# Kernel optimization log

Measured on AMD Instinct MI355X. Metric: run time of the kernel, lower is better.

## Reference

```python
import jax, jax.numpy as jnp
import numpy as np

D_MODEL = 2048
NUM_HEADS = 16
D_HEAD = D_MODEL // NUM_HEADS
MAX_SEQ_LEN = 2048
THETA = 10000.0


def setup_inputs() -> dict:
    key = jax.random.key(0)
    kx, kq, kk, kv, ko = jax.random.split(key, 5)
    std = float(np.sqrt(2.0 / (D_MODEL + D_MODEL)))
    def tn(k):
        # truncated normal in [-3std, 3std] scaled by std
        return std * jax.random.truncated_normal(k, -3.0, 3.0, (D_MODEL, D_MODEL), jnp.float32)
    return {
        "x": jax.random.normal(kx, (2, MAX_SEQ_LEN, D_MODEL), jnp.float32),
        "w_q": tn(kq),
        "w_k": tn(kk),
        "w_v": tn(kv),
        "w_o": tn(ko),
    }


def _rope(x):
    # x: [B, H, S, Dh], default positions = arange(S)
    S = x.shape[-2]
    pos = jnp.arange(S, dtype=jnp.float32)
    inv_freq = 1.0 / (THETA ** (jnp.arange(0, D_HEAD, 2, dtype=jnp.float32) / D_HEAD))
    ang = pos[:, None] * inv_freq[None, :]           # [S, Dh/2]
    cos = jnp.cos(ang).astype(x.dtype)
    sin = jnp.sin(ang).astype(x.dtype)
    x_even = x[..., 0::2]
    x_odd = x[..., 1::2]
    out_even = x_even * cos - x_odd * sin
    out_odd = x_even * sin + x_odd * cos
    # interleave even/odd back
    return jnp.stack([out_even, out_odd], axis=-1).reshape(x.shape)


def reference(x, w_q, w_k, w_v, w_o):
    B, S, _ = x.shape
    def split_heads(t):
        return t.reshape(B, S, NUM_HEADS, D_HEAD).transpose(0, 2, 1, 3)  # [B,H,S,Dh]
    q = split_heads(x @ w_q.T)
    k = split_heads(x @ w_k.T)
    v = split_heads(x @ w_v.T)
    q = _rope(q)
    k = _rope(k)
    scores = jnp.einsum('bhqd,bhkd->bhqk', q, k) / jnp.sqrt(jnp.asarray(D_HEAD, x.dtype))
    causal = jnp.tril(jnp.ones((S, S), dtype=bool))
    scores = jnp.where(causal, scores, jnp.finfo(scores.dtype).min)
    attn = jax.nn.softmax(scores, axis=-1)
    out = jnp.einsum('bhqk,bhkd->bhqd', attn, v)     # [B,H,S,Dh]
    out = out.transpose(0, 2, 1, 3).reshape(B, S, D_MODEL)
    return out @ w_o.T
```

## Files before the change

### kernel.cpp

```cpp
#include <hip/hip_runtime.h>
#include <hip/hip_bf16.h>

typedef __bf16 bf16;
typedef __bf16 bf16x8 __attribute__((ext_vector_type(8)));
typedef __bf16 bf16x4 __attribute__((ext_vector_type(4)));
typedef float f32x4 __attribute__((ext_vector_type(4)));

#define MFMA_BF16(a, b, c) __builtin_amdgcn_mfma_f32_16x16x32_bf16(a, b, c, 0, 0, 0)

constexpr int D_MODEL = 2048;
constexpr int NUM_HEADS = 16;
constexpr int D_HEAD = 128;
constexpr int SEQ = 2048;
constexpr int BATCH = 2;
constexpr int M_TOTAL = BATCH * SEQ;

__device__ __forceinline__ void gld_lds16(const bf16* g, bf16* l) {
  __builtin_amdgcn_global_load_lds((const __attribute__((address_space(1))) void*)g,
                                   (__attribute__((address_space(3))) void*)l, 16, 0, 0);
}

__global__ __launch_bounds__(256) void cvt_all(const float* __restrict__ x,
                                               const float* __restrict__ wq,
                                               const float* __restrict__ wk,
                                               const float* __restrict__ wv,
                                               const float* __restrict__ wo,
                                               bf16* __restrict__ dst) {
  const long i = (long)blockIdx.x * 256 + threadIdx.x;
  const float* src;
  long off;
  if (i < 2097152) {
    src = x; off = i;
  } else {
    const long j = i - 2097152;
    const int w = (int)(j >> 20);
    off = j & 1048575;
    src = (w == 0) ? wq : (w == 1) ? wk : (w == 2) ? wv : wo;
  }
  float4 v = reinterpret_cast<const float4*>(src)[off];
  bf16x4 o;
  o[0] = (bf16)v.x; o[1] = (bf16)v.y; o[2] = (bf16)v.z; o[3] = (bf16)v.w;
  reinterpret_cast<bf16x4*>(dst)[i] = o;
}

enum { EP_F32 = 0, EP_QKV = 1 };

template <int EPI>
__global__ __launch_bounds__(512, 2) void gemm_bt(const bf16* __restrict__ A,
                                                  const bf16* __restrict__ B,
                                                  void* __restrict__ C0,
                                                  void* __restrict__ C1,
                                                  void* __restrict__ C2,
                                                  int M, int N, int K) {
  __shared__ __align__(16) bf16 As[3][256 * 32];
  __shared__ __align__(16) bf16 Bs[3][256 * 32];
  const int tid = threadIdx.x;
  const int lane = tid & 63;
  const int wave = tid >> 6;
  const int lane15 = lane & 15;
  const int quad = lane >> 4;

  const int nwg = gridDim.x;
  const int cpx = nwg >> 3;
  const int swz = (blockIdx.x & 7) * cpx + (blockIdx.x >> 3);
  const int NBX = N >> 8;
  const int m0 = (swz / NBX) * 256;
  const int n0 = (swz % NBX) * 256;

  const int wm = (wave >> 2) * 128;
  const int wn = (wave & 3) * 64;

  const int arow = wave * 16 + (lane >> 2);
  const int achk = ((lane & 3) ^ (arow & 3)) * 8;
  long a_off[2], b_off[2];
#pragma unroll
  for (int i = 0; i < 2; ++i) {
    a_off[i] = (long)(m0 + i * 128 + arow) * K + achk;
    b_off[i] = (long)(n0 + i * 128 + arow) * K + achk;
  }
  const int dstoff = wave * 512;

  const int ca = (quad ^ (lane15 & 3)) * 8;

  f32x4 acc[8][4];
#pragma unroll
  for (int i = 0; i < 8; ++i)
#pragma unroll
    for (int j = 0; j < 4; ++j) acc[i][j] = (f32x4){0.f, 0.f, 0.f, 0.f};

  const int NT = K >> 5;

#pragma unroll
  for (int i = 0; i < 2; ++i) gld_lds16(A + a_off[i], &As[0][i * 4096 + dstoff]);
#pragma unroll
  for (int i = 0; i < 2; ++i) gld_lds16(B + b_off[i], &Bs[0][i * 4096 + dstoff]);
#pragma unroll
  for (int i = 0; i < 2; ++i) gld_lds16(A + a_off[i] + 32, &As[1][i * 4096 + dstoff]);
#pragma unroll
  for (int i = 0; i < 2; ++i) gld_lds16(B + b_off[i] + 32, &Bs[1][i * 4096 + dstoff]);
  asm volatile("s_waitcnt vmcnt(4)" ::: "memory");
  __builtin_amdgcn_s_barrier();
  __builtin_amdgcn_sched_barrier(0);

  int bcur = 0, bstg = 2;
  for (int t = 0; t < NT; ++t) {
    const bf16* Ab = As[bcur];
    const bf16* Bb = Bs[bcur];
    const long kst = (long)(t + 2) * 32;
    const bool st = (t + 2 < NT);

    bf16x8 bfrg[4], afrg[4];
#pragma unroll
    for (int j = 0; j < 4; ++j)
      bfrg[j] = *reinterpret_cast<const bf16x8*>(&Bb[(wn + j * 16 + lane15) * 32 + ca]);
#pragma unroll
    for (int i = 0; i < 4; ++i)
      afrg[i] = *reinterpret_cast<const bf16x8*>(&Ab[(wm + i * 16 + lane15) * 32 + ca]);
    if (st) {
      gld_lds16(A + a_off[0] + kst, &As[bstg][dstoff]);
      gld_lds16(A + a_off[1] + kst, &As[bstg][4096 + dstoff]);
    }
    __builtin_amdgcn_s_barrier();
    __builtin_amdgcn_sched_barrier(0);
    __builtin_amdgcn_s_setprio(1);
#pragma unroll
    for (int i = 0; i < 4; ++i)
#pragma unroll
      for (int j = 0; j < 4; ++j) acc[i][j] = MFMA_BF16(afrg[i], bfrg[j], acc[i][j]);
    __builtin_amdgcn_s_setprio(0);

    bf16x8 afr2[4];
#pragma unroll
    for (int i = 0; i < 4; ++i)
      afr2[i] = *reinterpret_cast<const bf16x8*>(&Ab[(wm + (i + 4) * 16 + lane15) * 32 + ca]);
    if (st) {
      gld_lds16(B + b_off[0] + kst, &Bs[bstg][dstoff]);
      gld_lds16(B + b_off[1] + kst, &Bs[bstg][4096 + dstoff]);
      asm volatile("s_waitcnt vmcnt(4)" ::: "memory");
    } else if (t == NT - 2) {
      asm volatile("s_waitcnt vmcnt(0)" ::: "memory");
    }
    __builtin_amdgcn_s_barrier();
    __builtin_amdgcn_sched_barrier(0);
    __builtin_amdgcn_s_setprio(1);
#pragma unroll
    for (int i = 0; i < 4; ++i)
#pragma unroll
      for (int j = 0; j < 4; ++j) acc[i + 4][j] = MFMA_BF16(afr2[i], bfrg[j], acc[i + 4][j]);
    __builtin_amdgcn_s_setprio(0);

    __builtin_amdgcn_s_barrier();
    __builtin_amdgcn_sched_barrier(0);
    bstg = bcur;
    bcur = (bcur == 2) ? 0 : bcur + 1;
  }

  if (EPI == EP_F32) {
#pragma unroll
    for (int i = 0; i < 8; ++i)
#pragma unroll
      for (int j = 0; j < 4; ++j)
#pragma unroll
        for (int r = 0; r < 4; ++r) {
          const int m = m0 + wm + i * 16 + quad * 4 + r;
          const int n = n0 + wn + j * 16 + lane15;
          reinterpret_cast<float*>(C0)[(long)m * N + n] = acc[i][j][r];
        }
  } else {
    const int mat = n0 >> 11;
    bf16* dst = (mat == 0) ? (bf16*)C0 : (mat == 1) ? (bf16*)C1 : (bf16*)C2;
    const int nb = n0 & 2047;
    if (mat < 2) {
#pragma unroll
      for (int i = 0; i < 8; ++i)
#pragma unroll
        for (int j = 0; j < 4; ++j)
#pragma unroll
          for (int r = 0; r < 4; ++r) {
            const int m = m0 + wm + i * 16 + quad * 4 + r;
            const int nl = nb + wn + j * 16 + lane15;
            const int b = m >> 11;
            const int s = m & (SEQ - 1);
            const int h = nl >> 7;
            const int d = nl & (D_HEAD - 1);
            float v = acc[i][j][r];
            float other = __shfl_xor(v, 1);
            float fr = exp2f((float)(d & ~1) * -0.103810253f);
            float ang = (float)s * fr;
            float sn = __sinf(ang);
            float cs = __cosf(ang);
            float outv = (lane15 & 1) ? (v * cs + other * sn) : (v * cs - other * sn);
            dst[(((long)(b * NUM_HEADS + h)) * SEQ + s) * D_HEAD + d] = (bf16)outv;
          }
    } else {
#pragma unroll
      for (int i = 0; i < 8; ++i)
#pragma unroll
        for (int j = 0; j < 4; ++j) {
          bf16x4 pk;
#pragma unroll
          for (int r = 0; r < 4; ++r) pk[r] = (bf16)acc[i][j][r];
          const int m = m0 + wm + i * 16 + quad * 4;
          const int b = m >> 11;
          const int s = m & (SEQ - 1);
          const int nl = nb + wn + j * 16 + lane15;
          const int h = nl >> 7;
          const int d = nl & (D_HEAD - 1);
          *reinterpret_cast<bf16x4*>(
              &dst[(((long)(b * NUM_HEADS + h)) * D_HEAD + d) * SEQ + s]) = pk;
        }
    }
  }
}

__global__ __launch_bounds__(256) void flash_attn(const bf16* __restrict__ Q,
                                                  const bf16* __restrict__ K,
                                                  const bf16* __restrict__ Vt,
                                                  bf16* __restrict__ O) {
  __shared__ __align__(16) bf16 Kl[2][64 * 128];
  __shared__ __align__(16) bf16 Vl[2][128 * 64];
  __shared__ __align__(16) bf16 P[4 * 16 * 72];
  const int tid = threadIdx.x;
  const int lane = tid & 63;
  const int wave = tid >> 6;
  const int lane15 = lane & 15;
  const int quad = lane >> 4;
  const int idx = blockIdx.x >> 3;
  const int bh = (blockIdx.x & 7) * 4 + (idx & 3);
  const int qcg = 31 - (idx >> 2);
  const int q0 = qcg * 64 + wave * 16;
  const long base = (long)bh * SEQ * D_HEAD;
  const bf16* qp = Q + base;
  const bf16* kp = K + base;
  const bf16* vp = Vt + base;
  bf16* Pw = &P[wave * 16 * 72];
  constexpr float scale = 0.08838834764831845f;
  constexpr float SMAX = 30.0f;

  int ksrc[4], vsrc[4];
  const int kdst = wave * 512;
#pragma unroll
  for (int i = 0; i < 4; ++i) {
    const int c = i * 256 + tid;
    const int krow = c >> 4;
    ksrc[i] = krow * D_HEAD + (((c & 15) ^ (krow & 15)) * 8);
    const int vd = c >> 3;
    vsrc[i] = vd * SEQ + (((c & 7) ^ (vd & 7)) * 8);
  }

  bf16x8 bq[4];
#pragma unroll
  for (int kk = 0; kk < 4; ++kk)
    bq[kk] = *reinterpret_cast<const bf16x8*>(qp + (long)(q0 + lane15) * D_HEAD + kk * 32 + quad * 8);

  f32x4 o_acc[8];
#pragma unroll
  for (int dj = 0; dj < 8; ++dj) o_acc[dj] = (f32x4){0.f, 0.f, 0.f, 0.f};
  float l_part = 0.f;
  const int qcol = q0 + lane15;

  const int nkt = qcg + 1;

#pragma unroll
  for (int i = 0; i < 4; ++i) gld_lds16(kp + ksrc[i], &Kl[0][i * 2048 + kdst]);
#pragma unroll
  for (int i = 0; i < 4; ++i) gld_lds16(vp + vsrc[i], &Vl[0][i * 2048 + kdst]);
  __syncthreads();

  for (int kt = 0; kt < nkt; ++kt) {
    const int k0 = kt * 64;
    const int buf = kt & 1;

    if (kt + 1 < nkt) {
      const int nk0 = k0 + 64;
#pragma unroll
      for (int i = 0; i < 4; ++i) gld_lds16(kp + nk0 * D_HEAD + ksrc[i], &Kl[buf ^ 1][i * 2048 + kdst]);
#pragma unroll
      for (int i = 0; i < 4; ++i) gld_lds16(vp + nk0 + vsrc[i], &Vl[buf ^ 1][i * 2048 + kdst]);
    }

    f32x4 sc[4];
#pragma unroll
    for (int j = 0; j < 4; ++j) sc[j] = (f32x4){0.f, 0.f, 0.f, 0.f};
#pragma unroll
    for (int j = 0; j < 4; ++j) {
#pragma unroll
      for (int kk = 0; kk < 4; ++kk) {
        bf16x8 ak = *reinterpret_cast<const bf16x8*>(
            &Kl[buf][(j * 16 + lane15) * D_HEAD + (((kk * 4 + quad) ^ lane15) * 8)]);
        sc[j] = MFMA_BF16(ak, bq[kk], sc[j]);
      }
    }

#pragma unroll
    for (int j = 0; j < 4; ++j) {
      bf16x4 pk;
#pragma unroll
      for (int r = 0; r < 4; ++r) {
        const int kpos = k0 + j * 16 + quad * 4 + r;
        float p = (kpos <= qcol) ? __expf(sc[j][r] * scale - SMAX) : 0.f;
        l_part += p;
        pk[r] = (bf16)p;
      }
      *reinterpret_cast<bf16x4*>(&Pw[lane15 * 72 + j * 16 + quad * 4]) = pk;
    }

#pragma unroll
    for (int kc = 0; kc < 2; ++kc) {
      bf16x8 ap = *reinterpret_cast<const bf16x8*>(&Pw[lane15 * 72 + kc * 32 + quad * 8]);
#pragma unroll
      for (int dj = 0; dj < 8; ++dj) {
        bf16x8 bv = *reinterpret_cast<const bf16x8*>(
            &Vl[buf][(dj * 16 + lane15) * 64 + (((kc * 4 + quad) ^ (lane15 & 7)) * 8)]);
        o_acc[dj] = MFMA_BF16(ap, bv, o_acc[dj]);
      }
    }

    __syncthreads();
  }

  float lsum = l_part;
  lsum += __shfl_xor(lsum, 16);
  lsum += __shfl_xor(lsum, 32);

  const int b = bh >> 4;
  const int h = bh & 15;
#pragma unroll
  for (int r = 0; r < 4; ++r) {
    const float lr = __shfl(lsum, quad * 4 + r);
    const float inv_l = 1.0f / lr;
    const int qrow = q0 + quad * 4 + r;
#pragma unroll
    for (int dj = 0; dj < 8; ++dj)
      O[((long)b * SEQ + qrow) * D_MODEL + h * D_HEAD + dj * 16 + lane15] =
          (bf16)(o_acc[dj][r] * inv_l);
  }
}

extern "C" void kernel_launch(void* const* d_in, const int* in_sizes, int n_in,
                              void* d_out, int out_size, void* d_ws, size_t ws_size,
                              hipStream_t stream) {
  const float* x = (const float*)d_in[0];
  const float* wq = (const float*)d_in[1];
  const float* wk = (const float*)d_in[2];
  const float* wv = (const float*)d_in[3];
  const float* wo = (const float*)d_in[4];
  float* out = (float*)d_out;

  char* ws = (char*)d_ws;
  size_t off = 0;
  bf16* x_bf = (bf16*)(ws + off);  off += (size_t)M_TOTAL * D_MODEL * 2;
  bf16* wq_bf = (bf16*)(ws + off); off += (size_t)D_MODEL * D_MODEL * 2;
  bf16* wk_bf = (bf16*)(ws + off); off += (size_t)D_MODEL * D_MODEL * 2;
  bf16* wv_bf = (bf16*)(ws + off); off += (size_t)D_MODEL * D_MODEL * 2;
  bf16* wo_bf = (bf16*)(ws + off); off += (size_t)D_MODEL * D_MODEL * 2;
  bf16* q_r = (bf16*)(ws + off);   off += (size_t)M_TOTAL * D_MODEL * 2;
  bf16* k_r = (bf16*)(ws + off);   off += (size_t)M_TOTAL * D_MODEL * 2;
  bf16* vt_r = (bf16*)(ws + off);  off += (size_t)M_TOTAL * D_MODEL * 2;
  bf16* a_o = (bf16*)(ws + off);   off += (size_t)M_TOTAL * D_MODEL * 2;

  cvt_all<<<24576, dim3(256), 0, stream>>>(x, wq, wk, wv, wo, x_bf);

  gemm_bt<EP_QKV><<<dim3((M_TOTAL / 256) * (3 * D_MODEL / 256)), dim3(512), 0, stream>>>(
      x_bf, wq_bf, q_r, k_r, vt_r, M_TOTAL, 3 * D_MODEL, D_MODEL);

  flash_attn<<<dim3(1024), dim3(256), 0, stream>>>(q_r, k_r, vt_r, a_o);

  gemm_bt<EP_F32><<<dim3((M_TOTAL / 256) * (D_MODEL / 256)), dim3(512), 0, stream>>>(
      a_o, wo_bf, out, nullptr, nullptr, M_TOTAL, D_MODEL, D_MODEL);
}
```

Baseline: 388.2 us.

## Template GEMM on M-tile, use 128-row tiles for output projection, simplify pipeline

Makes the GEMM kernel's M tile a template parameter. The output projection now uses 128-row tiles, which doubles its block count so the grid fills all CUs on the device. The main loop is restructured: all A and B prefetches are issued together, and the two half-MFMA phases with their intermediate barriers are collapsed into one phase. The LDS swizzle pattern is also changed. In exchange, register pressure rises in the 256-row instantiation, and the output GEMM loses some reuse of B per block.

```diff
diff --git a/kernel.cpp b/kernel.cpp
--- a/kernel.cpp
+++ b/kernel.cpp
@@ -45,14 +45,16 @@
 
 enum { EP_F32 = 0, EP_QKV = 1 };
 
-template <int EPI>
+template <int EPI, int BM>
 __global__ __launch_bounds__(512, 2) void gemm_bt(const bf16* __restrict__ A,
                                                   const bf16* __restrict__ B,
                                                   void* __restrict__ C0,
                                                   void* __restrict__ C1,
                                                   void* __restrict__ C2,
                                                   int M, int N, int K) {
-  __shared__ __align__(16) bf16 As[3][256 * 32];
+  constexpr int MFR = BM / 32;
+  constexpr int AI = BM / 128;
+  __shared__ __align__(16) bf16 As[3][BM * 32];
   __shared__ __align__(16) bf16 Bs[3][256 * 32];
   const int tid = threadIdx.x;
   const int lane = tid & 63;
@@ -64,41 +66,44 @@
   const int cpx = nwg >> 3;
   const int swz = (blockIdx.x & 7) * cpx + (blockIdx.x >> 3);
   const int NBX = N >> 8;
-  const int m0 = (swz / NBX) * 256;
+  const int m0 = (swz / NBX) * BM;
   const int n0 = (swz % NBX) * 256;
 
-  const int wm = (wave >> 2) * 128;
+  const int wm = (wave >> 2) * (BM / 2);
   const int wn = (wave & 3) * 64;
 
-  const int arow = wave * 16 + (lane >> 2);
-  const int achk = ((lane & 3) ^ (arow & 3)) * 8;
+  const int arow = tid >> 2;
+  const int achk = ((tid & 3) ^ ((arow >> 1) & 3)) * 8;
   long a_off[2], b_off[2];
 #pragma unroll
-  for (int i = 0; i < 2; ++i) {
-    a_off[i] = (long)(m0 + i * 128 + arow) * K + achk;
-    b_off[i] = (long)(n0 + i * 128 + arow) * K + achk;
-  }
+  for (int i = 0; i < AI; ++i) a_off[i] = (long)(m0 + i * 128 + arow) * K + achk;
+#pragma unroll
+  for (int i = 0; i < 2; ++i) b_off[i] = (long)(n0 + i * 128 + arow) * K + achk;
   const int dstoff = wave * 512;
 
-  const int ca = (quad ^ (lane15 & 3)) * 8;
-
-  f32x4 acc[8][4];
-#pragma unroll
-  for (int i = 0; i < 8; ++i)
+  const int ca = (quad ^ ((lane15 >> 1) & 3)) * 8;
+
+  f32x4 acc[MFR][4];
+#pragma unroll
+  for (int i = 0; i < MFR; ++i)
 #pragma unroll
     for (int j = 0; j < 4; ++j) acc[i][j] = (f32x4){0.f, 0.f, 0.f, 0.f};
 
   const int NT = K >> 5;
 
 #pragma unroll
-  for (int i = 0; i < 2; ++i) gld_lds16(A + a_off[i], &As[0][i * 4096 + dstoff]);
+  for (int i = 0; i < AI; ++i) gld_lds16(A + a_off[i], &As[0][i * 4096 + dstoff]);
 #pragma unroll
   for (int i = 0; i < 2; ++i) gld_lds16(B + b_off[i], &Bs[0][i * 4096 + dstoff]);
 #pragma unroll
-  for (int i = 0; i < 2; ++i) gld_lds16(A + a_off[i] + 32, &As[1][i * 4096 + dstoff]);
+  for (int i = 0; i < AI; ++i) gld_lds16(A + a_off[i] + 32, &As[1][i * 4096 + dstoff]);
 #pragma unroll
   for (int i = 0; i < 2; ++i) gld_lds16(B + b_off[i] + 32, &Bs[1][i * 4096 + dstoff]);
-  asm volatile("s_waitcnt vmcnt(4)" ::: "memory");
+  if constexpr (BM == 256) {
+    asm volatile("s_waitcnt vmcnt(4)" ::: "memory");
+  } else {
+    asm volatile("s_waitcnt vmcnt(3)" ::: "memory");
+  }
   __builtin_amdgcn_s_barrier();
   __builtin_amdgcn_sched_barrier(0);
 
@@ -109,46 +114,37 @@
     const long kst = (long)(t + 2) * 32;
     const bool st = (t + 2 < NT);
 
-    bf16x8 bfrg[4], afrg[4];
+    bf16x8 bfrg[4], afrg[MFR];
 #pragma unroll
     for (int j = 0; j < 4; ++j)
       bfrg[j] = *reinterpret_cast<const bf16x8*>(&Bb[(wn + j * 16 + lane15) * 32 + ca]);
 #pragma unroll
-    for (int i = 0; i < 4; ++i)
+    for (int i = 0; i < MFR; ++i)
       afrg[i] = *reinterpret_cast<const bf16x8*>(&Ab[(wm + i * 16 + lane15) * 32 + ca]);
+
     if (st) {
-      gld_lds16(A + a_off[0] + kst, &As[bstg][dstoff]);
-      gld_lds16(A + a_off[1] + kst, &As[bstg][4096 + dstoff]);
-    }
-    __builtin_amdgcn_s_barrier();
-    __builtin_amdgcn_sched_barrier(0);
+#pragma unroll
+      for (int i = 0; i < AI; ++i) gld_lds16(A + a_off[i] + kst, &As[bstg][i * 4096 + dstoff]);
+#pragma unroll
+      for (int i = 0; i < 2; ++i) gld_lds16(B + b_off[i] + kst, &Bs[bstg][i * 4096 + dstoff]);
+    }
+
     __builtin_amdgcn_s_setprio(1);
 #pragma unroll
-    for (int i = 0; i < 4; ++i)
+    for (int i = 0; i < MFR; ++i)
 #pragma unroll
       for (int j = 0; j < 4; ++j) acc[i][j] = MFMA_BF16(afrg[i], bfrg[j], acc[i][j]);
     __builtin_amdgcn_s_setprio(0);
 
-    bf16x8 afr2[4];
-#pragma unroll
-    for (int i = 0; i < 4; ++i)
-      afr2[i] = *reinterpret_cast<const bf16x8*>(&Ab[(wm + (i + 4) * 16 + lane15) * 32 + ca]);
     if (st) {
-      gld_lds16(B + b_off[0] + kst, &Bs[bstg][dstoff]);
-      gld_lds16(B + b_off[1] + kst, &Bs[bstg][4096 + dstoff]);
-      asm volatile("s_waitcnt vmcnt(4)" ::: "memory");
+      if constexpr (BM == 256) {
+        asm volatile("s_waitcnt vmcnt(4)" ::: "memory");
+      } else {
+        asm volatile("s_waitcnt vmcnt(3)" ::: "memory");
+      }
     } else if (t == NT - 2) {
       asm volatile("s_waitcnt vmcnt(0)" ::: "memory");
     }
-    __builtin_amdgcn_s_barrier();
-    __builtin_amdgcn_sched_barrier(0);
-    __builtin_amdgcn_s_setprio(1);
-#pragma unroll
-    for (int i = 0; i < 4; ++i)
-#pragma unroll
-      for (int j = 0; j < 4; ++j) acc[i + 4][j] = MFMA_BF16(afr2[i], bfrg[j], acc[i + 4][j]);
-    __builtin_amdgcn_s_setprio(0);
-
     __builtin_amdgcn_s_barrier();
     __builtin_amdgcn_sched_barrier(0);
     bstg = bcur;
@@ -157,7 +153,7 @@
 
   if (EPI == EP_F32) {
 #pragma unroll
-    for (int i = 0; i < 8; ++i)
+    for (int i = 0; i < MFR; ++i)
 #pragma unroll
       for (int j = 0; j < 4; ++j)
 #pragma unroll
@@ -172,7 +168,7 @@
     const int nb = n0 & 2047;
     if (mat < 2) {
 #pragma unroll
-      for (int i = 0; i < 8; ++i)
+      for (int i = 0; i < MFR; ++i)
 #pragma unroll
         for (int j = 0; j < 4; ++j)
 #pragma unroll
@@ -194,7 +190,7 @@
           }
     } else {
 #pragma unroll
-      for (int i = 0; i < 8; ++i)
+      for (int i = 0; i < MFR; ++i)
 #pragma unroll
         for (int j = 0; j < 4; ++j) {
           bf16x4 pk;
@@ -361,11 +357,11 @@
 
   cvt_all<<<24576, dim3(256), 0, stream>>>(x, wq, wk, wv, wo, x_bf);
 
-  gemm_bt<EP_QKV><<<dim3((M_TOTAL / 256) * (3 * D_MODEL / 256)), dim3(512), 0, stream>>>(
+  gemm_bt<EP_QKV, 256><<<dim3((M_TOTAL / 256) * (3 * D_MODEL / 256)), dim3(512), 0, stream>>>(
       x_bf, wq_bf, q_r, k_r, vt_r, M_TOTAL, 3 * D_MODEL, D_MODEL);
 
   flash_attn<<<dim3(1024), dim3(256), 0, stream>>>(q_r, k_r, vt_r, a_o);
 
-  gemm_bt<EP_F32><<<dim3((M_TOTAL / 256) * (D_MODEL / 256)), dim3(512), 0, stream>>>(
+  gemm_bt<EP_F32, 128><<<dim3((M_TOTAL / 128) * (D_MODEL / 256)), dim3(512), 0, stream>>>(
       a_o, wo_bf, out, nullptr, nullptr, M_TOTAL, D_MODEL, D_MODEL);
 }
```

New measurement: 364.6 us. 6.1% less time.
